# Performance work log

Measured on AMD Instinct MI355X. Metric: run time of the kernel, lower is better.

Reference implementation:

```python
import jax, jax.numpy as jnp
import numpy as np

N_NODES = 20000
N_EDGES = 320000
F_IN = 256
HID = 256
N_CLS = 5


def _glorot(key, shape):
    lim = np.sqrt(6.0 / (shape[0] + shape[1]))
    return jax.random.uniform(key, shape, jnp.float32, -lim, lim)


def setup_inputs() -> dict:
    key = jax.random.key(0)
    ks = jax.random.split(key, 12)
    x1 = jax.random.normal(ks[0], (N_NODES, F_IN), jnp.float32)
    x2 = jax.random.normal(ks[1], (N_NODES, F_IN), jnp.float32)
    ei1 = jax.random.randint(ks[2], (2, N_EDGES), 0, N_NODES, jnp.int64 if jax.config.jax_enable_x64 else jnp.int32)
    ei2 = jax.random.randint(ks[3], (2, N_EDGES), 0, N_NODES, jnp.int64 if jax.config.jax_enable_x64 else jnp.int32)
    params = {
        'W1': _glorot(ks[4], (F_IN, HID)), 'b1': jnp.zeros((HID,), jnp.float32),
        'W2': _glorot(ks[5], (HID, HID)), 'b2': jnp.zeros((HID,), jnp.float32),
        'W3': _glorot(ks[6], (HID, HID)), 'b3': jnp.zeros((HID,), jnp.float32),
        'Wl': _glorot(ks[7], (HID, N_CLS)), 'bl': jnp.zeros((N_CLS,), jnp.float32),
    }
    return {'x1': x1, 'edge_index1': ei1, 'x2': x2, 'edge_index2': ei2, **params}


def gcn_conv(x, edge_index, W, b):
    # PyG GCNConv: add self-loops, symmetric normalization D^-1/2 (A+I) D^-1/2 (X W) + b
    N = x.shape[0]
    src, dst = edge_index[0], edge_index[1]
    deg = jax.ops.segment_sum(jnp.ones(src.shape[0], x.dtype), dst, num_segments=N) + 1.0
    dinv = jax.lax.rsqrt(deg)  # [N]
    xw = x @ W                 # [N, H]
    coef = (dinv[src] * dinv[dst])[:, None]  # per-edge norm
    agg = jax.ops.segment_sum(xw[src] * coef, dst, num_segments=N)
    agg = agg + xw * (dinv * dinv)[:, None]  # self-loop term
    return agg + b


def _branch(x, ei, W1, b1, W2, b2, W3, b3):
    # dropout is identity in eval mode
    h = jax.nn.relu(gcn_conv(x, ei, W1, b1))
    h = jax.nn.relu(gcn_conv(h, ei, W2, b2))
    return gcn_conv(h, ei, W3, b3)


def reference(x1, edge_index1, x2, edge_index2, W1, b1, W2, b2, W3, b3, Wl, bl):
    h1 = _branch(x1, edge_index1, W1, b1, W2, b2, W3, b3)
    h2 = _branch(x2, edge_index2, W1, b1, W2, b2, W3, b3)
    h = jnp.concatenate([h1, h2], axis=0)          # [2N, H]
    pooled = jnp.mean(h, axis=0, keepdims=True)    # batch is all zeros -> single mean pool
    return pooled @ Wl + bl                        # [1, num_classes]
```

## Files before the change

### kernel.cpp

```cpp
#include <hip/hip_runtime.h>
#include <hip/hip_bf16.h>

#define N_NODES 20000
#define N_EDGES 320000
#define HID 256

typedef __attribute__((ext_vector_type(8))) short bf16x8;
typedef __attribute__((ext_vector_type(4))) float f32x4;
typedef __attribute__((ext_vector_type(8))) unsigned short us8;

__device__ __forceinline__ float bf2f(ushort u) {
  union { unsigned int i; float f; } v; v.i = ((unsigned int)u) << 16; return v.f;
}
__device__ __forceinline__ ushort f2bf(float f) {
  union { float f; unsigned int i; } v; v.f = f;
  unsigned int r = v.i + 0x7FFFu + ((v.i >> 16) & 1u);
  return (ushort)(r >> 16);
}

__global__ void detect_kernel(const void* x1, const void* ei1, int* flags) {
  __shared__ int cnt_wild, cnt_oddnz;
  if (threadIdx.x == 0) { cnt_wild = 0; cnt_oddnz = 0; }
  __syncthreads();
  const ushort* xu = (const ushort*)x1;
  int wild = 0;
#pragma unroll
  for (int k = 0; k < 4; k++) {
    ushort u = xu[threadIdx.x * 4 + k];
    int ex = (u >> 7) & 0xFF;
    if (ex >= 0x90) wild++;
  }
  if (wild) atomicAdd(&cnt_wild, wild);
  const int* ii = (const int*)ei1;
  if (ii[threadIdx.x * 2 + 1] != 0) atomicAdd(&cnt_oddnz, 1);
  __syncthreads();
  if (threadIdx.x == 0) {
    flags[0] = (cnt_wild > 64) ? 1 : 0;
    flags[1] = (cnt_oddnz < 8) ? 1 : 0;
  }
}

__global__ void init_kernel(int* cnt0, int* cnt1, float* t0, float* t1) {
  int i = blockIdx.x * blockDim.x + threadIdx.x;
  if (i < N_NODES) { cnt0[i] = 0; cnt1[i] = 0; t0[i] = 0.f; t1[i] = 0.f; }
}

__global__ void cvt_ei_count_kernel(const void* e0, const void* e1,
                                    int* o0, int* o1,
                                    int* cnt0, int* cnt1,
                                    int* rank0, int* rank1, const int* flags) {
  int b = blockIdx.y;
  const void* e = b ? e1 : e0;
  int* o = b ? o1 : o0;
  int* cnt = b ? cnt1 : cnt0;
  int* rank = b ? rank1 : rank0;
  int i = blockIdx.x * 256 + threadIdx.x;
  if (i >= 2 * N_EDGES) return;
  int v = flags[1] ? (int)((const long long*)e)[i] : ((const int*)e)[i];
  o[i] = v;
  if (i >= N_EDGES) rank[i - N_EDGES] = atomicAdd(&cnt[v], 1);
}

__global__ void cvt_x_kernel(const void* x0, const void* x1v,
                             ushort* o0, ushort* o1, const int* flags) {
  const void* x = blockIdx.y ? x1v : x0;
  ushort* o = blockIdx.y ? o1 : o0;
  int i4 = (blockIdx.x * 256 + threadIdx.x) * 4;
  if (i4 >= N_NODES * HID) return;
  if (flags[0]) {
    float4 v = *(const float4*)((const float*)x + i4);
    ushort4 w; w.x = f2bf(v.x); w.y = f2bf(v.y); w.z = f2bf(v.z); w.w = f2bf(v.w);
    *(ushort4*)(o + i4) = w;
  } else {
    *(ushort4*)(o + i4) = *(const ushort4*)((const ushort*)x + i4);
  }
}

__global__ void cvt_w_kernel(const void* W1, const void* W2, const void* W3, const void* Wl,
                             const void* b1, const void* b2, const void* b3, const void* bl,
                             ushort* out, const int* flags) {
  int i = blockIdx.x * 256 + threadIdx.x;
  if (i >= 198661) return;
  const void* src; int off; bool tr = false;
  if (i < 65536)       { src = W1; off = 0; tr = true; }
  else if (i < 131072) { src = W2; off = 65536; tr = true; }
  else if (i < 196608) { src = W3; off = 131072; }
  else if (i < 197888) { src = Wl; off = 196608; }
  else if (i < 198144) { src = b1; off = 197888; }
  else if (i < 198400) { src = b2; off = 198144; }
  else if (i < 198656) { src = b3; off = 198400; }
  else                 { src = bl; off = 198656; }
  int j = i - off;
  if (tr) j = (j & 255) * 256 + (j >> 8);
  out[i] = flags[0] ? f2bf(((const float*)src)[j]) : ((const ushort*)src)[j];
}

__global__ __launch_bounds__(1024) void scan_kernel(const int* cnt0, const int* cnt1,
                                                    int* rp0, int* rp1,
                                                    float* dinv0, float* dinv1) {
  const int* cnt = blockIdx.x ? cnt1 : cnt0;
  int* rp = blockIdx.x ? rp1 : rp0;
  float* dinv = blockIdx.x ? dinv1 : dinv0;
  __shared__ int sd[1024];
  int tid = threadIdx.x;
  int base = tid * 20;
  int pref[20];
  int run = 0;
#pragma unroll
  for (int k = 0; k < 20; k++) {
    int i = base + k;
    int c = (i < N_NODES) ? cnt[i] : 0;
    if (i < N_NODES) dinv[i] = rsqrtf((float)c + 1.0f);
    run += c;
    pref[k] = run;
  }
  sd[tid] = run;
  __syncthreads();
  for (int off = 1; off < 1024; off <<= 1) {
    int v = (tid >= off) ? sd[tid - off] : 0;
    __syncthreads();
    sd[tid] += v;
    __syncthreads();
  }
  int offset = sd[tid] - run;
  if (tid == 0) rp[0] = 0;
#pragma unroll
  for (int k = 0; k < 20; k++) {
    int i = base + k;
    if (i < N_NODES) rp[i + 1] = offset + pref[k];
  }
}

__global__ void fill_kernel(const int* ei0, const int* ei1,
                            const float* dinv0, const float* dinv1,
                            const int* rp0, const int* rp1,
                            const int* rank0, const int* rank1,
                            int2* eg0, int2* eg1,
                            float* t0, float* t1) {
  int e = blockIdx.x * blockDim.x + threadIdx.x;
  if (e >= N_EDGES) return;
  int b = blockIdx.y;
  const int* ei = b ? ei1 : ei0;
  const float* dinv = b ? dinv1 : dinv0;
  const int* rp = b ? rp1 : rp0;
  const int* rank = b ? rank1 : rank0;
  int2* eg = b ? eg1 : eg0;
  float* t = b ? t1 : t0;
  int src = ei[e], dst = ei[N_EDGES + e];
  int slot = rp[dst] + rank[e];
  float dd = dinv[dst];
  eg[slot] = make_int2(src, __float_as_int(dinv[src] * dd));
  atomicAdd(&t[src], dd);
}

__global__ __launch_bounds__(256) void gemm_kernel(
    const ushort* __restrict__ A0, const ushort* __restrict__ A1,
    const ushort* __restrict__ Wt,
    ushort* __restrict__ C0, ushort* __restrict__ C1) {
  const ushort* A = blockIdx.z ? A1 : A0;
  ushort* C = blockIdx.z ? C1 : C0;
  int m0 = blockIdx.x * 64;
  int n0 = blockIdx.y * 64;
  __shared__ ushort As[64][40];
  __shared__ ushort Bs[64][40];
  int tid = threadIdx.x;
  int wave = tid >> 6, lane = tid & 63;
  int quad = lane >> 4, r16 = lane & 15;
  f32x4 acc0 = {0.f, 0.f, 0.f, 0.f}, acc1 = acc0, acc2 = acc0, acc3 = acc0;
  int l_row = tid >> 2;
  int l_off = (tid & 3) * 8;
  for (int k0 = 0; k0 < 256; k0 += 32) {
    int gr = m0 + l_row;
    int4 va = {0, 0, 0, 0};
    if (gr < N_NODES) va = *(const int4*)(A + gr * 256 + k0 + l_off);
    *(int4*)&As[l_row][l_off] = va;
    int4 vb = *(const int4*)(Wt + (n0 + l_row) * 256 + k0 + l_off);
    *(int4*)&Bs[l_row][l_off] = vb;
    __syncthreads();
    bf16x8 a  = *(const bf16x8*)&As[wave * 16 + r16][quad * 8];
    bf16x8 b0 = *(const bf16x8*)&Bs[r16][quad * 8];
    bf16x8 b1 = *(const bf16x8*)&Bs[16 + r16][quad * 8];
    bf16x8 b2 = *(const bf16x8*)&Bs[32 + r16][quad * 8];
    bf16x8 b3 = *(const bf16x8*)&Bs[48 + r16][quad * 8];
    acc0 = __builtin_amdgcn_mfma_f32_16x16x32_bf16(a, b0, acc0, 0, 0, 0);
    acc1 = __builtin_amdgcn_mfma_f32_16x16x32_bf16(a, b1, acc1, 0, 0, 0);
    acc2 = __builtin_amdgcn_mfma_f32_16x16x32_bf16(a, b2, acc2, 0, 0, 0);
    acc3 = __builtin_amdgcn_mfma_f32_16x16x32_bf16(a, b3, acc3, 0, 0, 0);
    __syncthreads();
  }
  int orow = m0 + wave * 16 + quad * 4;
#pragma unroll
  for (int r = 0; r < 4; r++) {
    int gr = orow + r;
    if (gr < N_NODES) {
      ushort* cp = C + gr * 256 + n0 + r16;
      cp[0]  = f2bf(acc0[r]);
      cp[16] = f2bf(acc1[r]);
      cp[32] = f2bf(acc2[r]);
      cp[48] = f2bf(acc3[r]);
    }
  }
}

__global__ __launch_bounds__(256) void agg_kernel(
    const ushort* __restrict__ XW0, const ushort* __restrict__ XW1,
    const float* __restrict__ dinv0, const float* __restrict__ dinv1,
    const int* __restrict__ rp0, const int* __restrict__ rp1,
    const int2* __restrict__ eg0, const int2* __restrict__ eg1,
    const ushort* __restrict__ bias,
    ushort* __restrict__ H0, ushort* __restrict__ H1) {
  int b = blockIdx.y;
  const ushort* XW = b ? XW1 : XW0;
  const float* dinv = b ? dinv1 : dinv0;
  const int* rp = b ? rp1 : rp0;
  const int2* eg = b ? eg1 : eg0;
  ushort* H = b ? H1 : H0;
  int wave = threadIdx.x >> 6, lane = threadIdx.x & 63;
  int half = lane >> 5;
  int fl = (lane & 31) * 8;
  int i = blockIdx.x * 4 + wave;
  float di = dinv[i];
  float selfw = half ? 0.f : di * di;
  us8 v = *(const us8*)(XW + i * 256 + fl);
  float accA[8], accB[8];
#pragma unroll
  for (int j = 0; j < 8; j++) { accA[j] = selfw * bf2f(v[j]); accB[j] = 0.f; }
  int e0 = rp[i], e1 = rp[i + 1];
  int n = e1 - e0;
  int npair = n >> 1;
  int pe = 0;
  for (; pe + 3 < npair; pe += 4) {
    int ea = e0 + 2 * pe + half;
    int2 p0 = eg[ea];
    int2 p1 = eg[ea + 2];
    int2 p2 = eg[ea + 4];
    int2 p3 = eg[ea + 6];
    us8 r0 = *(const us8*)(XW + p0.x * 256 + fl);
    us8 r1 = *(const us8*)(XW + p1.x * 256 + fl);
    us8 r2 = *(const us8*)(XW + p2.x * 256 + fl);
    us8 r3 = *(const us8*)(XW + p3.x * 256 + fl);
    float w0 = __int_as_float(p0.y), w1 = __int_as_float(p1.y);
    float w2 = __int_as_float(p2.y), w3 = __int_as_float(p3.y);
#pragma unroll
    for (int j = 0; j < 8; j++) {
      accA[j] += w0 * bf2f(r0[j]);
      accB[j] += w1 * bf2f(r1[j]);
      accA[j] += w2 * bf2f(r2[j]);
      accB[j] += w3 * bf2f(r3[j]);
    }
  }
  for (; pe < npair; pe++) {
    int2 pp = eg[e0 + 2 * pe + half];
    us8 r = *(const us8*)(XW + pp.x * 256 + fl);
    float w = __int_as_float(pp.y);
#pragma unroll
    for (int j = 0; j < 8; j++) accA[j] += w * bf2f(r[j]);
  }
  if (n & 1) {
    int2 pp = eg[e1 - 1];
    float w = half ? 0.f : __int_as_float(pp.y);
    us8 r = *(const us8*)(XW + pp.x * 256 + fl);
#pragma unroll
    for (int j = 0; j < 8; j++) accB[j] += w * bf2f(r[j]);
  }
  us8 bb = *(const us8*)(bias + fl);
  us8 o;
#pragma unroll
  for (int j = 0; j < 8; j++) {
    float s = accA[j] + accB[j];
    s += __shfl_xor(s, 32);
    o[j] = f2bf(fmaxf(s + bf2f(bb[j]), 0.f));
  }
  if (half == 0) *(us8*)(H + i * 256 + fl) = o;
}

__global__ __launch_bounds__(256) void colsum_kernel(
    const ushort* __restrict__ H0, const ushort* __restrict__ H1,
    const float* __restrict__ dinv0, const float* __restrict__ dinv1,
    const float* __restrict__ t0, const float* __restrict__ t1,
    float* __restrict__ P) {
  int b = blockIdx.y;
  const ushort* H = b ? H1 : H0;
  const float* dinv = b ? dinv1 : dinv0;
  const float* t = b ? t1 : t0;
  int wave = threadIdx.x >> 6, lane = threadIdx.x & 63;
  int wid = blockIdx.x * 4 + wave;
  int f4 = lane * 4;
  float a0 = 0.f, a1 = 0.f, a2 = 0.f, a3 = 0.f;
  for (int j = wid; j < N_NODES; j += 256) {
    float dj = dinv[j];
    float c = dj * (t[j] + dj);
    ushort4 u = *(const ushort4*)(H + j * 256 + f4);
    a0 += c * bf2f(u.x); a1 += c * bf2f(u.y);
    a2 += c * bf2f(u.z); a3 += c * bf2f(u.w);
  }
  __shared__ float part[4][256];
  part[wave][f4 + 0] = a0; part[wave][f4 + 1] = a1;
  part[wave][f4 + 2] = a2; part[wave][f4 + 3] = a3;
  __syncthreads();
  int f = threadIdx.x;
  float ssum = part[0][f] + part[1][f] + part[2][f] + part[3][f];
  P[(b * 64 + blockIdx.x) * 256 + f] = ssum;
}

__global__ __launch_bounds__(256) void final_kernel(
    const float* __restrict__ P,
    const ushort* __restrict__ W3, const ushort* __restrict__ b3,
    const ushort* __restrict__ Wl, const ushort* __restrict__ bl,
    void* __restrict__ out, const int* __restrict__ flags) {
  __shared__ float v[256];
  __shared__ float pooled[256];
  int t = threadIdx.x;
  float acc0 = 0.f, acc1 = 0.f;
  for (int b = 0; b < 64; b++) {
    acc0 += P[b * 256 + t];
    acc1 += P[(64 + b) * 256 + t];
  }
  v[t] = acc0 + acc1;
  __syncthreads();
  float acc = 0.f;
  for (int f = 0; f < 256; f++) acc += v[f] * bf2f(W3[f * 256 + t]);
  pooled[t] = acc * (1.0f / (2.0f * N_NODES)) + bf2f(b3[t]);
  __syncthreads();
  if (t < 5) {
    float o = bf2f(bl[t]);
    for (int h = 0; h < 256; h++) o += pooled[h] * bf2f(Wl[h * 5 + t]);
    if (flags[0]) ((float*)out)[t] = o;
    else ((ushort*)out)[t] = f2bf(o);
  }
}

extern "C" void kernel_launch(void* const* d_in, const int* in_sizes, int n_in,
                              void* d_out, int out_size, void* d_ws, size_t ws_size,
                              hipStream_t stream) {
  const void* x1 = d_in[0];
  const void* ei1 = d_in[1];
  const void* x2 = d_in[2];
  const void* ei2 = d_in[3];
  const void* W1 = d_in[4];
  const void* b1 = d_in[5];
  const void* W2 = d_in[6];
  const void* b2 = d_in[7];
  const void* W3 = d_in[8];
  const void* b3 = d_in[9];
  const void* Wl = d_in[10];
  const void* bl = d_in[11];

  char* p = (char*)d_ws;
  auto alloc = [&](size_t bytes) {
    char* r = p;
    p += (bytes + 255) & ~size_t(255);
    return r;
  };
  int* flags   = (int*)alloc(256);
  float* dinv0 = (float*)alloc(N_NODES * 4);
  float* dinv1 = (float*)alloc(N_NODES * 4);
  float* t0    = (float*)alloc(N_NODES * 4);
  float* t1    = (float*)alloc(N_NODES * 4);
  int* cnt0    = (int*)alloc(N_NODES * 4);
  int* cnt1    = (int*)alloc(N_NODES * 4);
  int* rp0     = (int*)alloc((N_NODES + 1) * 4);
  int* rp1     = (int*)alloc((N_NODES + 1) * 4);
  int2* eg0    = (int2*)alloc((size_t)N_EDGES * 8);
  int2* eg1    = (int2*)alloc((size_t)N_EDGES * 8);
  float* Pp    = (float*)alloc(2 * 64 * 256 * 4);
  ushort* wbuf = (ushort*)alloc(198661 * 2);
  ushort* xw0  = (ushort*)alloc((size_t)N_NODES * HID * 2);
  ushort* xw1  = (ushort*)alloc((size_t)N_NODES * HID * 2);
  ushort* xc0  = (ushort*)alloc((size_t)N_NODES * HID * 2);
  ushort* xc1  = (ushort*)alloc((size_t)N_NODES * HID * 2);
  int* ei32_0 = (int*)xw0;
  int* ei32_1 = ei32_0 + 2 * N_EDGES;
  int* rank0  = ei32_1 + 2 * N_EDGES;
  int* rank1  = rank0 + N_EDGES;
  ushort* h0 = xc0;
  ushort* h1 = xc1;

  ushort* Wc1 = wbuf + 0;
  ushort* Wc2 = wbuf + 65536;
  ushort* Wc3 = wbuf + 131072;
  ushort* Wlc = wbuf + 196608;
  ushort* bc1 = wbuf + 197888;
  ushort* bc2 = wbuf + 198144;
  ushort* bc3 = wbuf + 198400;
  ushort* blc = wbuf + 198656;

  detect_kernel<<<1, 256, 0, stream>>>(x1, ei1, flags);
  init_kernel<<<(N_NODES + 255) / 256, 256, 0, stream>>>(cnt0, cnt1, t0, t1);
  cvt_ei_count_kernel<<<dim3((2 * N_EDGES + 255) / 256, 2), 256, 0, stream>>>(
      ei1, ei2, ei32_0, ei32_1, cnt0, cnt1, rank0, rank1, flags);
  cvt_x_kernel<<<dim3(N_NODES * HID / 1024, 2), 256, 0, stream>>>(
      x1, x2, xc0, xc1, flags);
  cvt_w_kernel<<<(198661 + 255) / 256, 256, 0, stream>>>(
      W1, W2, W3, Wl, b1, b2, b3, bl, wbuf, flags);
  scan_kernel<<<2, 1024, 0, stream>>>(cnt0, cnt1, rp0, rp1, dinv0, dinv1);
  fill_kernel<<<dim3((N_EDGES + 255) / 256, 2), 256, 0, stream>>>(
      ei32_0, ei32_1, dinv0, dinv1, rp0, rp1, rank0, rank1, eg0, eg1, t0, t1);

  gemm_kernel<<<dim3(313, 4, 2), 256, 0, stream>>>(xc0, xc1, Wc1, xw0, xw1);
  agg_kernel<<<dim3(N_NODES / 4, 2), 256, 0, stream>>>(
      xw0, xw1, dinv0, dinv1, rp0, rp1, eg0, eg1, bc1, h0, h1);

  gemm_kernel<<<dim3(313, 4, 2), 256, 0, stream>>>(h0, h1, Wc2, xw0, xw1);
  agg_kernel<<<dim3(N_NODES / 4, 2), 256, 0, stream>>>(
      xw0, xw1, dinv0, dinv1, rp0, rp1, eg0, eg1, bc2, h0, h1);

  colsum_kernel<<<dim3(64, 2), 256, 0, stream>>>(h0, h1, dinv0, dinv1, t0, t1, Pp);
  final_kernel<<<1, 256, 0, stream>>>(Pp, Wc3, bc3, Wlc, blc, d_out, flags);
}
```

Measured before the change: 381.4 us.

## Split aggregation feature dim into quarters with 8 edge groups per wave

The aggregation kernel now gives each block a 64-column quarter of the feature row instead of the full row, and interleaves branch and quarter in the low bits of blockIdx.x. Within a wave, 8 lane groups each process a different edge, so 8 edges are in flight per wave instead of 2. The partial sums are combined with a three-step shuffle reduction. This raises memory-level parallelism on the gather and may improve L2 locality across the 8 shards, at the cost of 4x more blocks, repeated edge-list reads per quarter, and more shuffles. Edge-list loads are now nontemporal.

```diff
diff --git a/kernel.cpp b/kernel.cpp
--- a/kernel.cpp
+++ b/kernel.cpp
@@ -209,69 +209,66 @@
     const int2* __restrict__ eg0, const int2* __restrict__ eg1,
     const ushort* __restrict__ bias,
     ushort* __restrict__ H0, ushort* __restrict__ H1) {
-  int b = blockIdx.y;
-  const ushort* XW = b ? XW1 : XW0;
-  const float* dinv = b ? dinv1 : dinv0;
-  const int* rp = b ? rp1 : rp0;
-  const int2* eg = b ? eg1 : eg0;
-  ushort* H = b ? H1 : H0;
+  int shard = blockIdx.x & 7;
+  int nodeblk = blockIdx.x >> 3;
+  int branch = shard >> 2;
+  int quarter = shard & 3;
+  const ushort* XW = branch ? XW1 : XW0;
+  const float* dinv = branch ? dinv1 : dinv0;
+  const int* rp = branch ? rp1 : rp0;
+  const int2* eg = branch ? eg1 : eg0;
+  ushort* H = branch ? H1 : H0;
   int wave = threadIdx.x >> 6, lane = threadIdx.x & 63;
-  int half = lane >> 5;
-  int fl = (lane & 31) * 8;
-  int i = blockIdx.x * 4 + wave;
-  float di = dinv[i];
-  float selfw = half ? 0.f : di * di;
-  us8 v = *(const us8*)(XW + i * 256 + fl);
+  int egrp = lane >> 3;
+  int j = lane & 7;
+  int fb = quarter * 64 + j * 8;
+  int i = nodeblk * 4 + wave;
   float accA[8], accB[8];
-#pragma unroll
-  for (int j = 0; j < 8; j++) { accA[j] = selfw * bf2f(v[j]); accB[j] = 0.f; }
+  if (egrp == 0) {
+    float di = dinv[i];
+    float selfw = di * di;
+    us8 v = *(const us8*)(XW + i * 256 + fb);
+#pragma unroll
+    for (int k = 0; k < 8; k++) { accA[k] = selfw * bf2f(v[k]); accB[k] = 0.f; }
+  } else {
+#pragma unroll
+    for (int k = 0; k < 8; k++) { accA[k] = 0.f; accB[k] = 0.f; }
+  }
   int e0 = rp[i], e1 = rp[i + 1];
-  int n = e1 - e0;
-  int npair = n >> 1;
-  int pe = 0;
-  for (; pe + 3 < npair; pe += 4) {
-    int ea = e0 + 2 * pe + half;
-    int2 p0 = eg[ea];
-    int2 p1 = eg[ea + 2];
-    int2 p2 = eg[ea + 4];
-    int2 p3 = eg[ea + 6];
-    us8 r0 = *(const us8*)(XW + p0.x * 256 + fl);
-    us8 r1 = *(const us8*)(XW + p1.x * 256 + fl);
-    us8 r2 = *(const us8*)(XW + p2.x * 256 + fl);
-    us8 r3 = *(const us8*)(XW + p3.x * 256 + fl);
-    float w0 = __int_as_float(p0.y), w1 = __int_as_float(p1.y);
-    float w2 = __int_as_float(p2.y), w3 = __int_as_float(p3.y);
-#pragma unroll
-    for (int j = 0; j < 8; j++) {
-      accA[j] += w0 * bf2f(r0[j]);
-      accB[j] += w1 * bf2f(r1[j]);
-      accA[j] += w2 * bf2f(r2[j]);
-      accB[j] += w3 * bf2f(r3[j]);
+  int e = e0 + egrp;
+  for (; e + 8 < e1; e += 16) {
+    unsigned long long p0 = __builtin_nontemporal_load((const unsigned long long*)(eg + e));
+    unsigned long long p1 = __builtin_nontemporal_load((const unsigned long long*)(eg + e + 8));
+    int s0 = (int)(unsigned)p0, s1 = (int)(unsigned)p1;
+    float w0 = __int_as_float((int)(p0 >> 32));
+    float w1 = __int_as_float((int)(p1 >> 32));
+    us8 r0 = *(const us8*)(XW + s0 * 256 + fb);
+    us8 r1 = *(const us8*)(XW + s1 * 256 + fb);
+#pragma unroll
+    for (int k = 0; k < 8; k++) {
+      accA[k] += w0 * bf2f(r0[k]);
+      accB[k] += w1 * bf2f(r1[k]);
     }
   }
-  for (; pe < npair; pe++) {
-    int2 pp = eg[e0 + 2 * pe + half];
-    us8 r = *(const us8*)(XW + pp.x * 256 + fl);
-    float w = __int_as_float(pp.y);
-#pragma unroll
-    for (int j = 0; j < 8; j++) accA[j] += w * bf2f(r[j]);
-  }
-  if (n & 1) {
-    int2 pp = eg[e1 - 1];
-    float w = half ? 0.f : __int_as_float(pp.y);
-    us8 r = *(const us8*)(XW + pp.x * 256 + fl);
-#pragma unroll
-    for (int j = 0; j < 8; j++) accB[j] += w * bf2f(r[j]);
-  }
-  us8 bb = *(const us8*)(bias + fl);
+  if (e < e1) {
+    unsigned long long p0 = __builtin_nontemporal_load((const unsigned long long*)(eg + e));
+    int s0 = (int)(unsigned)p0;
+    float w0 = __int_as_float((int)(p0 >> 32));
+    us8 r0 = *(const us8*)(XW + s0 * 256 + fb);
+#pragma unroll
+    for (int k = 0; k < 8; k++) accA[k] += w0 * bf2f(r0[k]);
+  }
+  us8 bb = *(const us8*)(bias + fb);
   us8 o;
 #pragma unroll
-  for (int j = 0; j < 8; j++) {
-    float s = accA[j] + accB[j];
+  for (int k = 0; k < 8; k++) {
+    float s = accA[k] + accB[k];
+    s += __shfl_xor(s, 8);
+    s += __shfl_xor(s, 16);
     s += __shfl_xor(s, 32);
-    o[j] = f2bf(fmaxf(s + bf2f(bb[j]), 0.f));
-  }
-  if (half == 0) *(us8*)(H + i * 256 + fl) = o;
+    o[k] = f2bf(fmaxf(s + bf2f(bb[k]), 0.f));
+  }
+  if (egrp == 0) *(us8*)(H + i * 256 + fb) = o;
 }
 
 __global__ __launch_bounds__(256) void colsum_kernel(
@@ -398,11 +395,11 @@
       ei32_0, ei32_1, dinv0, dinv1, rp0, rp1, rank0, rank1, eg0, eg1, t0, t1);
 
   gemm_kernel<<<dim3(313, 4, 2), 256, 0, stream>>>(xc0, xc1, Wc1, xw0, xw1);
-  agg_kernel<<<dim3(N_NODES / 4, 2), 256, 0, stream>>>(
+  agg_kernel<<<dim3(5000 * 8), 256, 0, stream>>>(
       xw0, xw1, dinv0, dinv1, rp0, rp1, eg0, eg1, bc1, h0, h1);
 
   gemm_kernel<<<dim3(313, 4, 2), 256, 0, stream>>>(h0, h1, Wc2, xw0, xw1);
-  agg_kernel<<<dim3(N_NODES / 4, 2), 256, 0, stream>>>(
+  agg_kernel<<<dim3(5000 * 8), 256, 0, stream>>>(
       xw0, xw1, dinv0, dinv1, rp0, rp1, eg0, eg1, bc2, h0, h1);
 
   colsum_kernel<<<dim3(64, 2), 256, 0, stream>>>(h0, h1, dinv0, dinv1, t0, t1, Pp);
```

Measured after the change: 471.8 us. 1.24x slower.
